# Performance work log

Measured on AMD Instinct MI355X. Metric: run time of the kernel, lower is better.

## Reference

```python
import jax, jax.numpy as jnp
import numpy as np

# CSV_Architecture_v2 layout (per frame, 130 floats):
#   hand 0 block: [0]=handedness label, [1]=handedness prob, [2:65]=21*3 coords
#   hand 1 block: [65]=handedness label, [66]=handedness prob, [67:130]=coords
POS0, PROB0 = 0, 1
POS1, PROB1 = 65, 66
HAND_LEN = 65
FRAME_LEN = 2 * HAND_LEN


def _build_swap_pattern():
    all_idxs = np.arange(FRAME_LEN)
    idxs_0 = np.arange(0, HAND_LEN)
    idxs_1 = np.arange(HAND_LEN, FRAME_LEN)
    all_idxs[idxs_0], all_idxs[idxs_1] = all_idxs[idxs_1].copy(), all_idxs[idxs_0].copy()
    return jnp.asarray(all_idxs, dtype=jnp.int32)


def setup_inputs() -> dict:
    key = jax.random.key(0)
    B, S = 256, 1024
    X = jax.random.normal(key, (B, S, FRAME_LEN), dtype=jnp.float32)
    return {"X": X, "swap_pattern": _build_swap_pattern()}


def reference(X, swap_pattern):
    # Per-frame handedness labels / probabilities.
    h0 = X[..., POS0]
    h1 = X[..., POS1]
    p0 = X[..., PROB0]
    p1 = X[..., PROB1]

    nan0 = jnp.isnan(h0)
    nan1 = jnp.isnan(h1)
    no_nan = jnp.logical_and(~nan0, ~nan1)

    one = jnp.float32(1.0)
    zero = jnp.float32(0.0)

    # skip1: hands already ordered (right label > left label)
    skip1 = h1 > h0
    # skip2: both predictions NaN -> no hands detected
    skip2 = jnp.logical_and(nan0, nan1)
    # skip3: only hand 1 present, labeled right (==1)
    skip3 = jnp.logical_and(nan0, h1 == one)
    # skip4: only hand 0 present, labeled left (==0)
    skip4 = jnp.logical_and(nan1, h0 == zero)
    eq = h0 == h1
    # skip5: both labeled left, position-0 hand has higher prob
    skip5 = no_nan & eq & (h0 == zero) & (p0 > p1)
    # skip6: both labeled right, position-1 hand has higher prob
    skip6 = no_nan & eq & (h0 == one) & (p0 < p1)

    skip = skip1 | skip2 | skip3 | skip4 | skip5 | skip6

    # Vectorized replacement of nested tf.map_fn: gather-permute the frame
    # representation where a swap is required.
    swapped = X[..., swap_pattern]  # [B, S, FRAME_LEN]
    return jnp.where(skip[..., None], X, swapped)
```

## Files before the change

kernel.cpp:

```cpp
#include <hip/hip_runtime.h>

constexpr int FRAME_LEN = 130;
constexpr int HALF      = 65;
constexpr int BLOCK     = 256;
constexpr int FPB       = 32;
constexpr int CHUNK_F   = FPB * FRAME_LEN;

typedef float f4u __attribute__((ext_vector_type(4), aligned(4)));

__device__ __forceinline__ int div130(int idx) {
    return (int)(((unsigned)idx * 8067u) >> 20);
}

__global__ __launch_bounds__(BLOCK, 8)
void hand_sorter_kernel(const float* __restrict__ X, float* __restrict__ out,
                        int n_frames) {
    __shared__ int s_off[FPB];

    const int t = threadIdx.x;
    const long long frame0 = (long long)blockIdx.x * FPB;
    const long long rem = (long long)n_frames - frame0;
    const int frames_here = rem < (long long)FPB ? (int)rem : FPB;
    const int nf = frames_here * FRAME_LEN;
    const int n4 = (nf + 3) >> 2;
    const long long base = frame0 * (long long)FRAME_LEN;
    const float* __restrict__ Xb = X + base;
    float* __restrict__ Ob = out + base;

    if (t < frames_here) {
        const float* fr = Xb + t * FRAME_LEN;
        const float h0 = fr[0];
        const float p0 = fr[1];
        const float h1 = fr[HALF];
        const float p1 = fr[HALF + 1];
        const bool nan0 = (h0 != h0);
        const bool nan1 = (h1 != h1);
        const bool no_nan = !nan0 && !nan1;
        const bool eq = (h0 == h1);
        const bool skip =
            (h1 > h0) ||
            (nan0 && nan1) ||
            (nan0 && (h1 == 1.0f)) ||
            (nan1 && (h0 == 0.0f)) ||
            (no_nan && eq && (h0 == 0.0f) && (p0 > p1)) ||
            (no_nan && eq && (h0 == 1.0f) && (p0 < p1));
        s_off[t] = skip ? 0 : HALF;
    }
    __syncthreads();

    for (int i = t; i < n4; i += BLOCK) {
        const int idx = 4 * i;
        const int fl = div130(idx);
        const int jj = idx - fl * FRAME_LEN;
        const bool same_frame = (idx + 3 < nf) && (jj <= FRAME_LEN - 4);
        const bool no_half_cross = (jj < HALF - 3) || (jj >= HALF);
        if (same_frame && no_half_cross) {
            int sj = jj + s_off[fl];
            if (sj >= FRAME_LEN) sj -= FRAME_LEN;
            const float* src = Xb + (fl * FRAME_LEN + sj);
            f4u v = *(const f4u*)src;
            float4 o;
            o.x = v.x; o.y = v.y; o.z = v.z; o.w = v.w;
            *(float4*)(Ob + idx) = o;
        } else {
#pragma unroll
            for (int e = 0; e < 4; ++e) {
                const int ide = idx + e;
                if (ide < nf) {
                    const int fle = div130(ide);
                    const int je = ide - fle * FRAME_LEN;
                    int sj = je + s_off[fle];
                    if (sj >= FRAME_LEN) sj -= FRAME_LEN;
                    Ob[ide] = Xb[fle * FRAME_LEN + sj];
                }
            }
        }
    }
}

extern "C" void kernel_launch(void* const* d_in, const int* in_sizes, int n_in,
                              void* d_out, int out_size, void* d_ws, size_t ws_size,
                              hipStream_t stream) {
    const float* X = (const float*)d_in[0];
    float* out = (float*)d_out;
    const int n_frames = in_sizes[0] / FRAME_LEN;
    const int n_blocks = (n_frames + FPB - 1) / FPB;
    hand_sorter_kernel<<<n_blocks, BLOCK, 0, stream>>>(X, out, n_frames);
}
```

Baseline: 268.9 us.

## Stage full frame chunks in LDS with aligned float4 loads and stores

For full blocks, the kernel loads the 32-frame chunk with aligned float4 global loads issued up front, stages it in shared memory, and computes skip flags with a wave ballot into a bitmask. It then permutes from shared memory and writes back with aligned float4 stores. This removes the unaligned and scalar global accesses of the old gather loop. In exchange it uses about 16.6 KB of LDS per block, which may limit occupancy, and does scalar LDS reads with div130 index math per element. Partial tail blocks use a simple scalar path.

```diff
diff --git a/kernel.cpp b/kernel.cpp
--- a/kernel.cpp
+++ b/kernel.cpp
@@ -5,75 +5,112 @@
 constexpr int BLOCK     = 256;
 constexpr int FPB       = 32;
 constexpr int CHUNK_F   = FPB * FRAME_LEN;
-
-typedef float f4u __attribute__((ext_vector_type(4), aligned(4)));
+constexpr int N4        = CHUNK_F / 4;
 
 __device__ __forceinline__ int div130(int idx) {
     return (int)(((unsigned)idx * 8067u) >> 20);
 }
 
+__device__ __forceinline__ bool skip_pred(float h0, float p0, float h1, float p1) {
+    const bool nan0 = (h0 != h0);
+    const bool nan1 = (h1 != h1);
+    const bool no_nan = !nan0 && !nan1;
+    const bool eq = (h0 == h1);
+    return (h1 > h0) ||
+           (nan0 && nan1) ||
+           (nan0 && (h1 == 1.0f)) ||
+           (nan1 && (h0 == 0.0f)) ||
+           (no_nan && eq && (h0 == 0.0f) && (p0 > p1)) ||
+           (no_nan && eq && (h0 == 1.0f) && (p0 < p1));
+}
+
 __global__ __launch_bounds__(BLOCK, 8)
 void hand_sorter_kernel(const float* __restrict__ X, float* __restrict__ out,
                         int n_frames) {
-    __shared__ int s_off[FPB];
+    __shared__ float s_buf[CHUNK_F];
+    __shared__ unsigned s_mask;
 
     const int t = threadIdx.x;
     const long long frame0 = (long long)blockIdx.x * FPB;
     const long long rem = (long long)n_frames - frame0;
     const int frames_here = rem < (long long)FPB ? (int)rem : FPB;
-    const int nf = frames_here * FRAME_LEN;
-    const int n4 = (nf + 3) >> 2;
     const long long base = frame0 * (long long)FRAME_LEN;
     const float* __restrict__ Xb = X + base;
     float* __restrict__ Ob = out + base;
 
-    if (t < frames_here) {
-        const float* fr = Xb + t * FRAME_LEN;
-        const float h0 = fr[0];
-        const float p0 = fr[1];
-        const float h1 = fr[HALF];
-        const float p1 = fr[HALF + 1];
-        const bool nan0 = (h0 != h0);
-        const bool nan1 = (h1 != h1);
-        const bool no_nan = !nan0 && !nan1;
-        const bool eq = (h0 == h1);
-        const bool skip =
-            (h1 > h0) ||
-            (nan0 && nan1) ||
-            (nan0 && (h1 == 1.0f)) ||
-            (nan1 && (h0 == 0.0f)) ||
-            (no_nan && eq && (h0 == 0.0f) && (p0 > p1)) ||
-            (no_nan && eq && (h0 == 1.0f) && (p0 < p1));
-        s_off[t] = skip ? 0 : HALF;
-    }
-    __syncthreads();
+    if (frames_here == FPB) {
+        const float4* __restrict__ Xv = (const float4*)Xb;
+        float4* __restrict__ Ov = (float4*)Ob;
 
-    for (int i = t; i < n4; i += BLOCK) {
-        const int idx = 4 * i;
-        const int fl = div130(idx);
-        const int jj = idx - fl * FRAME_LEN;
-        const bool same_frame = (idx + 3 < nf) && (jj <= FRAME_LEN - 4);
-        const bool no_half_cross = (jj < HALF - 3) || (jj >= HALF);
-        if (same_frame && no_half_cross) {
-            int sj = jj + s_off[fl];
-            if (sj >= FRAME_LEN) sj -= FRAME_LEN;
-            const float* src = Xb + (fl * FRAME_LEN + sj);
-            f4u v = *(const f4u*)src;
-            float4 o;
-            o.x = v.x; o.y = v.y; o.z = v.z; o.w = v.w;
-            *(float4*)(Ob + idx) = o;
-        } else {
+        float4 r0 = Xv[t];
+        float4 r1 = Xv[t + 256];
+        float4 r2 = Xv[t + 512];
+        float4 r3 = Xv[t + 768];
+        float4 r4;
+        if (t < 16) r4 = Xv[t + 1024];
+
+        bool skip = false;
+        if (t < FPB) {
+            const float* fr = Xb + t * FRAME_LEN;
+            skip = skip_pred(fr[0], fr[1], fr[HALF], fr[HALF + 1]);
+        }
+        if (t < 64) {
+            unsigned long long b = __ballot(skip);
+            if (t == 0) s_mask = (unsigned)b;
+        }
+
+        *(float4*)(s_buf + 4 * t)         = r0;
+        *(float4*)(s_buf + 4 * (t + 256)) = r1;
+        *(float4*)(s_buf + 4 * (t + 512)) = r2;
+        *(float4*)(s_buf + 4 * (t + 768)) = r3;
+        if (t < 16) *(float4*)(s_buf + 4 * (t + 1024)) = r4;
+        __syncthreads();
+
+        const unsigned mask = s_mask;
+
+        float4 o[4];
+#pragma unroll
+        for (int k = 0; k < 4; ++k) {
+            const int idx = 4 * (t + k * 256);
+            float* op = (float*)&o[k];
 #pragma unroll
             for (int e = 0; e < 4; ++e) {
                 const int ide = idx + e;
-                if (ide < nf) {
-                    const int fle = div130(ide);
-                    const int je = ide - fle * FRAME_LEN;
-                    int sj = je + s_off[fle];
-                    if (sj >= FRAME_LEN) sj -= FRAME_LEN;
-                    Ob[ide] = Xb[fle * FRAME_LEN + sj];
-                }
+                const int fle = div130(ide);
+                const int je  = ide - fle * FRAME_LEN;
+                int sj = je + (((mask >> fle) & 1u) ? 0 : HALF);
+                if (sj >= FRAME_LEN) sj -= FRAME_LEN;
+                op[e] = s_buf[fle * FRAME_LEN + sj];
             }
+        }
+        float4 o4;
+        if (t < 16) {
+            const int idx = 4 * (t + 1024);
+            float* op = (float*)&o4;
+#pragma unroll
+            for (int e = 0; e < 4; ++e) {
+                const int ide = idx + e;
+                const int fle = div130(ide);
+                const int je  = ide - fle * FRAME_LEN;
+                int sj = je + (((mask >> fle) & 1u) ? 0 : HALF);
+                if (sj >= FRAME_LEN) sj -= FRAME_LEN;
+                op[e] = s_buf[fle * FRAME_LEN + sj];
+            }
+        }
+
+#pragma unroll
+        for (int k = 0; k < 4; ++k) Ov[t + k * 256] = o[k];
+        if (t < 16) Ov[t + 1024] = o4;
+    } else {
+        const int nf = frames_here * FRAME_LEN;
+        for (int i = t; i < nf; i += BLOCK) {
+            const int fle = div130(i);
+            const int je  = i - fle * FRAME_LEN;
+            const float* fr = Xb + fle * FRAME_LEN;
+            const bool skip = skip_pred(fr[0], fr[1], fr[HALF], fr[HALF + 1]);
+            int sj = je + (skip ? 0 : HALF);
+            if (sj >= FRAME_LEN) sj -= FRAME_LEN;
+            Ob[i] = fr[sj];
         }
     }
 }
```

New measurement: 237.5 us. -11.7%, faster.

## Replace LDS skip table with wave ballot and aligned vector loads with shuffles

Applied to the files above, without the earlier changes.

Each wave computes the per-frame skip predicates itself and packs them into a ballot mask, which removes the shared-memory table and the block barrier. Unaligned float4 source reads are replaced by two aligned 16-byte loads plus a lane shuffle, the loop is fully unrolled into five vector outputs per thread, and outputs use nontemporal stores. Occupancy bounds drop from 8 to 4 blocks per CU. Every wave redundantly reloads the frame header values, and each output now costs two loads instead of one, though these mostly hit cache.

```diff
diff --git a/kernel.cpp b/kernel.cpp
--- a/kernel.cpp
+++ b/kernel.cpp
@@ -5,75 +5,109 @@
 constexpr int BLOCK     = 256;
 constexpr int FPB       = 32;
 constexpr int CHUNK_F   = FPB * FRAME_LEN;
+constexpr int CHUNK_V4  = CHUNK_F / 4;
 
-typedef float f4u __attribute__((ext_vector_type(4), aligned(4)));
+typedef float v4f __attribute__((ext_vector_type(4)));
 
 __device__ __forceinline__ int div130(int idx) {
     return (int)(((unsigned)idx * 8067u) >> 20);
 }
 
-__global__ __launch_bounds__(BLOCK, 8)
+__device__ __forceinline__ bool skip_pred(float h0, float p0, float h1, float p1) {
+    const bool nan0 = (h0 != h0);
+    const bool nan1 = (h1 != h1);
+    const bool no_nan = !nan0 && !nan1;
+    const bool eq = (h0 == h1);
+    return (h1 > h0) ||
+           (nan0 && nan1) ||
+           (nan0 && (h1 == 1.0f)) ||
+           (nan1 && (h0 == 0.0f)) ||
+           (no_nan && eq && (h0 == 0.0f) && (p0 > p1)) ||
+           (no_nan && eq && (h0 == 1.0f) && (p0 < p1));
+}
+
+__device__ __forceinline__ v4f make_out(const v4f* __restrict__ Xv,
+                                        const float* __restrict__ Xb,
+                                        unsigned mask, int i) {
+    const int idx = 4 * i;
+    const int fl  = div130(idx);
+    const int jj  = idx - fl * FRAME_LEN;
+    const bool fast = (jj <= FRAME_LEN - 4) && (jj < HALF - 3 || jj >= HALF);
+    v4f r;
+    if (fast) {
+        const bool skipf = (mask >> fl) & 1u;
+        const bool lo = (jj < HALF);
+        const int s = idx + (skipf ? 0 : (lo ? HALF : -HALF));
+        const int a = s >> 2;
+        int a1 = a + 1;
+        if (a1 >= CHUNK_V4) a1 = CHUNK_V4 - 1;
+        const v4f va = Xv[a];
+        const v4f vb = Xv[a1];
+        v4f f1; f1.x = va.y; f1.y = va.z; f1.z = va.w; f1.w = vb.x;
+        v4f f3; f3.x = va.w; f3.y = vb.x; f3.z = vb.y; f3.w = vb.z;
+        const v4f swp = lo ? f1 : f3;
+        r = skipf ? va : swp;
+    } else {
+#pragma unroll
+        for (int e = 0; e < 4; ++e) {
+            const int ide = idx + e;
+            const int fle = div130(ide);
+            const int je  = ide - fle * FRAME_LEN;
+            const bool sk = (mask >> fle) & 1u;
+            int sj = je + (sk ? 0 : (je < HALF ? HALF : -HALF));
+            ((float*)&r)[e] = Xb[fle * FRAME_LEN + sj];
+        }
+    }
+    return r;
+}
+
+__global__ __launch_bounds__(BLOCK, 4)
 void hand_sorter_kernel(const float* __restrict__ X, float* __restrict__ out,
                         int n_frames) {
-    __shared__ int s_off[FPB];
-
     const int t = threadIdx.x;
     const long long frame0 = (long long)blockIdx.x * FPB;
     const long long rem = (long long)n_frames - frame0;
     const int frames_here = rem < (long long)FPB ? (int)rem : FPB;
-    const int nf = frames_here * FRAME_LEN;
-    const int n4 = (nf + 3) >> 2;
     const long long base = frame0 * (long long)FRAME_LEN;
     const float* __restrict__ Xb = X + base;
     float* __restrict__ Ob = out + base;
 
-    if (t < frames_here) {
-        const float* fr = Xb + t * FRAME_LEN;
-        const float h0 = fr[0];
-        const float p0 = fr[1];
-        const float h1 = fr[HALF];
-        const float p1 = fr[HALF + 1];
-        const bool nan0 = (h0 != h0);
-        const bool nan1 = (h1 != h1);
-        const bool no_nan = !nan0 && !nan1;
-        const bool eq = (h0 == h1);
-        const bool skip =
-            (h1 > h0) ||
-            (nan0 && nan1) ||
-            (nan0 && (h1 == 1.0f)) ||
-            (nan1 && (h0 == 0.0f)) ||
-            (no_nan && eq && (h0 == 0.0f) && (p0 > p1)) ||
-            (no_nan && eq && (h0 == 1.0f) && (p0 < p1));
-        s_off[t] = skip ? 0 : HALF;
-    }
-    __syncthreads();
+    if (frames_here == FPB) {
+        const int lane = t & 63;
+        bool pred = false;
+        if (lane < FPB) {
+            const float* fr = Xb + lane * FRAME_LEN;
+            const float2 a = *(const float2*)fr;
+            const float2 b = *(const float2*)(fr + 64);
+            const float2 c = *(const float2*)(fr + 66);
+            pred = skip_pred(a.x, a.y, b.y, c.x);
+        }
+        const unsigned mask = (unsigned)__ballot(pred);
 
-    for (int i = t; i < n4; i += BLOCK) {
-        const int idx = 4 * i;
-        const int fl = div130(idx);
-        const int jj = idx - fl * FRAME_LEN;
-        const bool same_frame = (idx + 3 < nf) && (jj <= FRAME_LEN - 4);
-        const bool no_half_cross = (jj < HALF - 3) || (jj >= HALF);
-        if (same_frame && no_half_cross) {
-            int sj = jj + s_off[fl];
-            if (sj >= FRAME_LEN) sj -= FRAME_LEN;
-            const float* src = Xb + (fl * FRAME_LEN + sj);
-            f4u v = *(const f4u*)src;
-            float4 o;
-            o.x = v.x; o.y = v.y; o.z = v.z; o.w = v.w;
-            *(float4*)(Ob + idx) = o;
-        } else {
-#pragma unroll
-            for (int e = 0; e < 4; ++e) {
-                const int ide = idx + e;
-                if (ide < nf) {
-                    const int fle = div130(ide);
-                    const int je = ide - fle * FRAME_LEN;
-                    int sj = je + s_off[fle];
-                    if (sj >= FRAME_LEN) sj -= FRAME_LEN;
-                    Ob[ide] = Xb[fle * FRAME_LEN + sj];
-                }
-            }
+        const v4f* __restrict__ Xv = (const v4f*)Xb;
+        v4f* __restrict__ Ov = (v4f*)Ob;
+
+        v4f o0 = make_out(Xv, Xb, mask, t);
+        v4f o1 = make_out(Xv, Xb, mask, t + 256);
+        v4f o2 = make_out(Xv, Xb, mask, t + 512);
+        v4f o3 = make_out(Xv, Xb, mask, t + 768);
+        __builtin_nontemporal_store(o0, Ov + t);
+        __builtin_nontemporal_store(o1, Ov + t + 256);
+        __builtin_nontemporal_store(o2, Ov + t + 512);
+        __builtin_nontemporal_store(o3, Ov + t + 768);
+        if (t < CHUNK_V4 - 1024) {
+            v4f o4 = make_out(Xv, Xb, mask, t + 1024);
+            __builtin_nontemporal_store(o4, Ov + t + 1024);
+        }
+    } else {
+        const int nf = frames_here * FRAME_LEN;
+        for (int i = t; i < nf; i += BLOCK) {
+            const int fle = div130(i);
+            const int je  = i - fle * FRAME_LEN;
+            const float* fr = Xb + fle * FRAME_LEN;
+            const bool sk = skip_pred(fr[0], fr[1], fr[HALF], fr[HALF + 1]);
+            int sj = je + (sk ? 0 : (je < HALF ? HALF : -HALF));
+            Ob[i] = fr[sj];
         }
     }
 }
```

Measured after the change: 242.3 us. 9.9% less time.
